# Optimization experiments

Hardware: AMD Instinct MI355X
Metric: run time of the kernel (lower is better)

## Reference

```python
import jax, jax.numpy as jnp
import numpy as np

IN_FEATURES = 4096
OUT_FEATURES = 16384
SCALE = 0.02


def setup_inputs() -> dict:
    key = jax.random.key(0)
    kx, kw, kb = jax.random.split(key, 3)
    x = jax.random.normal(kx, (4, 2048, IN_FEATURES), dtype=jnp.float32)
    # int8-valued quantized weight, stored as int32 (values in [-127, 127])
    q_weight = jax.random.randint(kw, (OUT_FEATURES, IN_FEATURES), -127, 128, dtype=jnp.int32)
    scale = jnp.float32(SCALE)
    bias = jax.random.normal(kb, (OUT_FEATURES,), dtype=jnp.float32)
    return {"x": x, "q_weight": q_weight, "scale": scale, "bias": bias}


def reference(x, q_weight, scale, bias):
    # weight = q_weight.float() * scale  (dequantize)
    weight = q_weight.astype(jnp.float32) * scale  # [out, in]
    # F.linear(x, weight, bias) = x @ weight.T + bias
    out = jnp.einsum('bsi,oi->bso', x, weight) + bias
    return out
```

## Files before the change

### kernel.cpp

```cpp
#include <hip/hip_runtime.h>
#include <stdint.h>

#define K_DIM 4096
#define N_DIM 16384
#define M_DIM 8192

typedef _Float16 half8 __attribute__((ext_vector_type(8)));
typedef float floatx4 __attribute__((ext_vector_type(4)));

__device__ inline void gld_lds16(const void* g, void* l) {
  __builtin_amdgcn_global_load_lds(
      (const __attribute__((address_space(1))) void*)g,
      (__attribute__((address_space(3))) void*)l, 16, 0, 0);
}

__global__ __launch_bounds__(256) void cvt_f32_f16_k(const float* __restrict__ in,
                                                     _Float16* __restrict__ out) {
  size_t idx = (size_t)blockIdx.x * 256 + threadIdx.x;
  const float4* p = (const float4*)in + idx * 2;
  float4 v0 = p[0], v1 = p[1];
  half8 h;
  h[0] = (_Float16)v0.x; h[1] = (_Float16)v0.y; h[2] = (_Float16)v0.z; h[3] = (_Float16)v0.w;
  h[4] = (_Float16)v1.x; h[5] = (_Float16)v1.y; h[6] = (_Float16)v1.z; h[7] = (_Float16)v1.w;
  *((half8*)out + idx) = h;
}

__global__ __launch_bounds__(256) void cvt_i32_f16_k(const int* __restrict__ in,
                                                     _Float16* __restrict__ out) {
  size_t idx = (size_t)blockIdx.x * 256 + threadIdx.x;
  const int4* p = (const int4*)in + idx * 2;
  int4 v0 = p[0], v1 = p[1];
  half8 h;
  h[0] = (_Float16)v0.x; h[1] = (_Float16)v0.y; h[2] = (_Float16)v0.z; h[3] = (_Float16)v0.w;
  h[4] = (_Float16)v1.x; h[5] = (_Float16)v1.y; h[6] = (_Float16)v1.z; h[7] = (_Float16)v1.w;
  *((half8*)out + idx) = h;
}

__global__ __launch_bounds__(512, 2) void qgemm256_k(
    const _Float16* __restrict__ Ah, const _Float16* __restrict__ Bh,
    const float* __restrict__ scale_p, const float* __restrict__ bias,
    float* __restrict__ out) {
  constexpr int BK = 64;
  constexpr int NT = K_DIM / BK;
  __shared__ __align__(16) _Float16 sA[2][256 * BK];
  __shared__ __align__(16) _Float16 sB[2][256 * BK];

  const int tid  = threadIdx.x;
  const int lane = tid & 63;
  const int wid  = tid >> 6;
  const int wm   = wid >> 2;
  const int wn   = wid & 3;
  const int q    = lane >> 4;
  const int l15  = lane & 15;

  const int nbn = N_DIM / 256;
  int lin = blockIdx.y * gridDim.x + blockIdx.x;
  int swz = (lin & 7) * ((M_DIM / 256) * nbn / 8) + (lin >> 3);
  const int bn = swz % nbn;
  const int bm = swz / nbn;

  const int s_slot = tid & 7;
  const int r0     = tid >> 3;
  const int cc     = s_slot ^ (r0 & 7);
  const _Float16* Agp = Ah + (size_t)(bm * 256 + r0) * K_DIM + cc * 8;
  const _Float16* Bgp = Bh + (size_t)(bn * 256 + r0) * K_DIM + cc * 8;

#define STAGE_A(b, tt, h)                                                        \
  { const _Float16* s_ = Agp + (size_t)(h) * 128 * K_DIM + (tt) * BK;            \
    gld_lds16(s_, &sA[(b)][(h) * 8192 + tid * 8]);                               \
    gld_lds16(s_ + (size_t)64 * K_DIM, &sA[(b)][(h) * 8192 + 4096 + tid * 8]); }
#define STAGE_B(b, tt, h)                                                        \
  { const _Float16* s_ = Bgp + (size_t)(h) * 128 * K_DIM + (tt) * BK;            \
    gld_lds16(s_, &sB[(b)][(h) * 8192 + tid * 8]);                               \
    gld_lds16(s_ + (size_t)64 * K_DIM, &sB[(b)][(h) * 8192 + 4096 + tid * 8]); }
#define MFMA16(d, a_, b_) d = __builtin_amdgcn_mfma_f32_16x16x32_f16(a_, b_, d, 0, 0, 0)
#define SBAR() __builtin_amdgcn_sched_barrier(0)
#define BARRIER() { SBAR(); __builtin_amdgcn_s_barrier(); SBAR(); }

  const int rbA = (wm * 128 + l15) * BK;
  const int rbB = (wn * 64 + l15) * BK;
  const int xt0 = (q ^ (l15 & 7)) * 8;
  const int xt1 = ((q + 4) ^ (l15 & 7)) * 8;

  floatx4 acc[8][4] = {};

  STAGE_A(0, 0, 0); STAGE_A(0, 0, 1);
  STAGE_B(0, 0, 0); STAGE_B(0, 0, 1);
  STAGE_A(1, 1, 0); STAGE_A(1, 1, 1);
  asm volatile("s_waitcnt vmcnt(4)" ::: "memory");
  BARRIER();

#pragma unroll 1
  for (int t = 0; t < NT; ++t) {
    const int buf = t & 1;
    const _Float16* pa = sA[buf];
    const _Float16* pb = sB[buf];
    half8 a0[8], a1[8], b0[4], b1[4];

    b0[0] = *(const half8*)&pb[rbB + xt0];
    b0[1] = *(const half8*)&pb[rbB + 1024 + xt0];
#pragma unroll
    for (int i = 0; i < 8; ++i) a0[i] = *(const half8*)&pa[rbA + i * 1024 + xt0];
    if (t < NT - 1) STAGE_B(buf ^ 1, t + 1, 0);
    BARRIER();
    __builtin_amdgcn_s_setprio(1);
#pragma unroll
    for (int i = 0; i < 8; ++i) { MFMA16(acc[i][0], a0[i], b0[0]); MFMA16(acc[i][1], a0[i], b0[1]); }
    __builtin_amdgcn_s_setprio(0);
    BARRIER();

    b0[2] = *(const half8*)&pb[rbB + 2048 + xt0];
    b0[3] = *(const half8*)&pb[rbB + 3072 + xt0];
#pragma unroll
    for (int i = 0; i < 8; ++i) a1[i] = *(const half8*)&pa[rbA + i * 1024 + xt1];
    if (t < NT - 1) STAGE_B(buf ^ 1, t + 1, 1);
    BARRIER();
    __builtin_amdgcn_s_setprio(1);
#pragma unroll
    for (int i = 0; i < 8; ++i) { MFMA16(acc[i][2], a0[i], b0[2]); MFMA16(acc[i][3], a0[i], b0[3]); }
    __builtin_amdgcn_s_setprio(0);
    BARRIER();

    b1[0] = *(const half8*)&pb[rbB + xt1];
    b1[1] = *(const half8*)&pb[rbB + 1024 + xt1];
    if (t < NT - 2) STAGE_A(buf, t + 2, 0);
    BARRIER();
    __builtin_amdgcn_s_setprio(1);
#pragma unroll
    for (int i = 0; i < 8; ++i) { MFMA16(acc[i][0], a1[i], b1[0]); MFMA16(acc[i][1], a1[i], b1[1]); }
    __builtin_amdgcn_s_setprio(0);
    BARRIER();

    b1[2] = *(const half8*)&pb[rbB + 2048 + xt1];
    b1[3] = *(const half8*)&pb[rbB + 3072 + xt1];
    if (t < NT - 2) STAGE_A(buf, t + 2, 1);
    BARRIER();
    __builtin_amdgcn_s_setprio(1);
#pragma unroll
    for (int i = 0; i < 8; ++i) { MFMA16(acc[i][2], a1[i], b1[2]); MFMA16(acc[i][3], a1[i], b1[3]); }
    __builtin_amdgcn_s_setprio(0);
    if (t < NT - 2) { asm volatile("s_waitcnt vmcnt(4)" ::: "memory"); }
    else            { asm volatile("s_waitcnt vmcnt(0)" ::: "memory"); }
    BARRIER();
  }

  const float s = *scale_p;
  float bv[4];
#pragma unroll
  for (int j = 0; j < 4; ++j) bv[j] = bias[bn * 256 + wn * 64 + j * 16 + l15];
  const int mb = bm * 256 + wm * 128 + q * 4;
  const size_t nb = (size_t)bn * 256 + wn * 64 + l15;
#pragma unroll
  for (int i = 0; i < 8; ++i) {
#pragma unroll
    for (int j = 0; j < 4; ++j) {
      size_t off = (size_t)(mb + i * 16) * N_DIM + nb + j * 16;
      floatx4 c = acc[i][j];
      out[off]             = c[0] * s + bv[j];
      out[off + N_DIM]     = c[1] * s + bv[j];
      out[off + 2 * N_DIM] = c[2] * s + bv[j];
      out[off + 3 * N_DIM] = c[3] * s + bv[j];
    }
  }
#undef STAGE_A
#undef STAGE_B
#undef MFMA16
#undef SBAR
#undef BARRIER
}

template <bool FROM_WS>
__global__ __launch_bounds__(256) void qgemm_k(const void* __restrict__ Av,
                                               const void* __restrict__ Bv,
                                               const float* __restrict__ scale_p,
                                               const float* __restrict__ bias,
                                               float* __restrict__ out) {
  constexpr int BK = 64;
  __shared__ __align__(16) _Float16 sA[128 * BK];
  __shared__ __align__(16) _Float16 sB[128 * BK];

  const int tid  = threadIdx.x;
  const int lane = tid & 63;
  const int wid  = tid >> 6;
  const int wm   = wid >> 1, wn = wid & 1;
  const int q    = lane >> 4;
  const int l15  = lane & 15;
  const int bn   = blockIdx.x, bm = blockIdx.y;

  int gI[4], rI[4], cI[4];
#pragma unroll
  for (int p = 0; p < 4; ++p) {
    int g = p * 256 + tid;
    gI[p] = g;
    rI[p] = g >> 3;
    cI[p] = (g & 7) ^ (rI[p] & 7);
  }

  floatx4 acc[4][4] = {};

  const int arow = wm * 64 + l15;
  const int brow = wn * 64 + l15;

  const _Float16* Ahp = nullptr; const _Float16* Bhp = nullptr;
  const float* Af = nullptr;     const int* Bq = nullptr;
  if constexpr (FROM_WS) { Ahp = (const _Float16*)Av; Bhp = (const _Float16*)Bv; }
  else                   { Af = (const float*)Av;     Bq = (const int*)Bv; }

#pragma unroll 1
  for (int k0 = 0; k0 < K_DIM; k0 += BK) {
    if constexpr (FROM_WS) {
#pragma unroll
      for (int p = 0; p < 4; ++p)
        gld_lds16(Ahp + (size_t)(bm * 128 + rI[p]) * K_DIM + k0 + cI[p] * 8, &sA[gI[p] * 8]);
#pragma unroll
      for (int p = 0; p < 4; ++p)
        gld_lds16(Bhp + (size_t)(bn * 128 + rI[p]) * K_DIM + k0 + cI[p] * 8, &sB[gI[p] * 8]);
    } else {
#pragma unroll
      for (int p = 0; p < 4; ++p) {
        const float4* pa =
            (const float4*)(Af + (size_t)(bm * 128 + rI[p]) * K_DIM + k0 + cI[p] * 8);
        float4 v0 = pa[0], v1 = pa[1];
        half8 h;
        h[0] = (_Float16)v0.x; h[1] = (_Float16)v0.y; h[2] = (_Float16)v0.z; h[3] = (_Float16)v0.w;
        h[4] = (_Float16)v1.x; h[5] = (_Float16)v1.y; h[6] = (_Float16)v1.z; h[7] = (_Float16)v1.w;
        *(half8*)&sA[gI[p] * 8] = h;
      }
#pragma unroll
      for (int p = 0; p < 4; ++p) {
        const int4* pb =
            (const int4*)(Bq + (size_t)(bn * 128 + rI[p]) * K_DIM + k0 + cI[p] * 8);
        int4 v0 = pb[0], v1 = pb[1];
        half8 h;
        h[0] = (_Float16)v0.x; h[1] = (_Float16)v0.y; h[2] = (_Float16)v0.z; h[3] = (_Float16)v0.w;
        h[4] = (_Float16)v1.x; h[5] = (_Float16)v1.y; h[6] = (_Float16)v1.z; h[7] = (_Float16)v1.w;
        *(half8*)&sB[gI[p] * 8] = h;
      }
    }
    __syncthreads();

#pragma unroll
    for (int kk = 0; kk < BK; kk += 32) {
      const int xt = ((((kk >> 3) + q) ^ (lane & 7)) * 8);
      half8 af[4], bf[4];
#pragma unroll
      for (int i = 0; i < 4; ++i) af[i] = *(const half8*)&sA[(arow + i * 16) * BK + xt];
#pragma unroll
      for (int j = 0; j < 4; ++j) bf[j] = *(const half8*)&sB[(brow + j * 16) * BK + xt];
#pragma unroll
      for (int i = 0; i < 4; ++i)
#pragma unroll
        for (int j = 0; j < 4; ++j)
          acc[i][j] = __builtin_amdgcn_mfma_f32_16x16x32_f16(af[i], bf[j], acc[i][j], 0, 0, 0);
    }
    __syncthreads();
  }

  const float s = *scale_p;
  float bv[4];
#pragma unroll
  for (int j = 0; j < 4; ++j) bv[j] = bias[bn * 128 + wn * 64 + j * 16 + l15];
  const int mb = bm * 128 + wm * 64 + q * 4;
  const size_t nb = (size_t)bn * 128 + wn * 64 + l15;
#pragma unroll
  for (int i = 0; i < 4; ++i) {
#pragma unroll
    for (int j = 0; j < 4; ++j) {
      size_t off = (size_t)(mb + i * 16) * N_DIM + nb + j * 16;
      floatx4 c = acc[i][j];
      out[off]             = c[0] * s + bv[j];
      out[off + N_DIM]     = c[1] * s + bv[j];
      out[off + 2 * N_DIM] = c[2] * s + bv[j];
      out[off + 3 * N_DIM] = c[3] * s + bv[j];
    }
  }
}

extern "C" void kernel_launch(void* const* d_in, const int* in_sizes, int n_in,
                              void* d_out, int out_size, void* d_ws, size_t ws_size,
                              hipStream_t stream) {
  const float* x     = (const float*)d_in[0];
  const int*   qw    = (const int*)d_in[1];
  const float* scale = (const float*)d_in[2];
  const float* bias  = (const float*)d_in[3];
  float* out = (float*)d_out;

  const size_t xs  = (size_t)M_DIM * K_DIM;
  const size_t wsz = (size_t)N_DIM * K_DIM;
  const size_t need = (xs + wsz) * sizeof(_Float16);

  if (ws_size >= need) {
    _Float16* xh = (_Float16*)d_ws;
    _Float16* wh = xh + xs;
    cvt_f32_f16_k<<<(int)(xs / 8 / 256), 256, 0, stream>>>(x, xh);
    cvt_i32_f16_k<<<(int)(wsz / 8 / 256), 256, 0, stream>>>(qw, wh);
    dim3 grid(N_DIM / 256, M_DIM / 256);
    qgemm256_k<<<grid, 512, 0, stream>>>(xh, wh, scale, bias, out);
  } else {
    dim3 grid(N_DIM / 128, M_DIM / 128);
    qgemm_k<false><<<grid, 256, 0, stream>>>(x, qw, scale, bias, out);
  }
}
```

Baseline: 1.827 ms.

## Restructure GEMM main loop into unrolled two-tile ping-pong with finer-grained staging

Unrolls the K loop by two so each half works on a fixed LDS buffer, and reorganizes the per-tile schedule. Each tile now issues all B fragment reads up front, splits A reads into quarter groups interleaved with 4x4 MFMA blocks, and spreads global-to-LDS staging of the next tiles across the phases using explicit lgkmcnt/vmcnt waits and raw s_barriers. The aim is better overlap of LDS reads, global loads and MFMA issue, and less scheduling overhead from sched_barriers. In exchange it holds more registers live and relies on hand-tuned wait counts, which could cause races or spills if the counts are wrong.

```diff
diff --git a/kernel.cpp b/kernel.cpp
--- a/kernel.cpp
+++ b/kernel.cpp
@@ -42,6 +42,7 @@
     float* __restrict__ out) {
   constexpr int BK = 64;
   constexpr int NT = K_DIM / BK;
+  constexpr int NI = NT / 2;
   __shared__ __align__(16) _Float16 sA[2][256 * BK];
   __shared__ __align__(16) _Float16 sB[2][256 * BK];
 
@@ -73,9 +74,23 @@
   { const _Float16* s_ = Bgp + (size_t)(h) * 128 * K_DIM + (tt) * BK;            \
     gld_lds16(s_, &sB[(b)][(h) * 8192 + tid * 8]);                               \
     gld_lds16(s_ + (size_t)64 * K_DIM, &sB[(b)][(h) * 8192 + 4096 + tid * 8]); }
-#define MFMA16(d, a_, b_) d = __builtin_amdgcn_mfma_f32_16x16x32_f16(a_, b_, d, 0, 0, 0)
-#define SBAR() __builtin_amdgcn_sched_barrier(0)
-#define BARRIER() { SBAR(); __builtin_amdgcn_s_barrier(); SBAR(); }
+#define MFMA_Q(i0, AARR, BARR)                                                   \
+  { _Pragma("unroll") for (int ii = 0; ii < 4; ++ii)                             \
+    _Pragma("unroll") for (int jj = 0; jj < 4; ++jj)                             \
+      acc[(i0) + ii][jj] = __builtin_amdgcn_mfma_f32_16x16x32_f16(               \
+          AARR[(i0) + ii], BARR[jj], acc[(i0) + ii][jj], 0, 0, 0); }
+#define RD_B4(arr, PB, XT)                                                       \
+  { _Pragma("unroll") for (int jj = 0; jj < 4; ++jj)                             \
+      arr[jj] = *(const half8*)&PB[rbB + jj * 1024 + (XT)]; }
+#define RD_A4(arr, i0, PA, XT)                                                   \
+  { _Pragma("unroll") for (int ii = 0; ii < 4; ++ii)                             \
+      arr[(i0) + ii] = *(const half8*)&PA[rbA + ((i0) + ii) * 1024 + (XT)]; }
+#define LGKM0()                                                                  \
+  { asm volatile("s_waitcnt lgkmcnt(0)" ::: "memory");                           \
+    __builtin_amdgcn_sched_barrier(0); }
+#define PRIO_MFMA(i0, AARR, BARR)                                                \
+  { __builtin_amdgcn_s_setprio(1); MFMA_Q(i0, AARR, BARR);                       \
+    __builtin_amdgcn_s_setprio(0); }
 
   const int rbA = (wm * 128 + l15) * BK;
   const int rbB = (wn * 64 + l15) * BK;
@@ -86,62 +101,82 @@
 
   STAGE_A(0, 0, 0); STAGE_A(0, 0, 1);
   STAGE_B(0, 0, 0); STAGE_B(0, 0, 1);
-  STAGE_A(1, 1, 0); STAGE_A(1, 1, 1);
-  asm volatile("s_waitcnt vmcnt(4)" ::: "memory");
-  BARRIER();
+  STAGE_B(1, 1, 0); STAGE_B(1, 1, 1);
+  STAGE_A(1, 1, 0);
+  asm volatile("s_waitcnt vmcnt(6)" ::: "memory");
+  __builtin_amdgcn_s_barrier();
 
 #pragma unroll 1
-  for (int t = 0; t < NT; ++t) {
-    const int buf = t & 1;
-    const _Float16* pa = sA[buf];
-    const _Float16* pb = sB[buf];
+  for (int i = 0; i < NI; ++i) {
+    const int t0 = 2 * i;
+    const bool more = (i < NI - 1);
     half8 a0[8], a1[8], b0[4], b1[4];
 
-    b0[0] = *(const half8*)&pb[rbB + xt0];
-    b0[1] = *(const half8*)&pb[rbB + 1024 + xt0];
-#pragma unroll
-    for (int i = 0; i < 8; ++i) a0[i] = *(const half8*)&pa[rbA + i * 1024 + xt0];
-    if (t < NT - 1) STAGE_B(buf ^ 1, t + 1, 0);
-    BARRIER();
-    __builtin_amdgcn_s_setprio(1);
-#pragma unroll
-    for (int i = 0; i < 8; ++i) { MFMA16(acc[i][0], a0[i], b0[0]); MFMA16(acc[i][1], a0[i], b0[1]); }
-    __builtin_amdgcn_s_setprio(0);
-    BARRIER();
-
-    b0[2] = *(const half8*)&pb[rbB + 2048 + xt0];
-    b0[3] = *(const half8*)&pb[rbB + 3072 + xt0];
-#pragma unroll
-    for (int i = 0; i < 8; ++i) a1[i] = *(const half8*)&pa[rbA + i * 1024 + xt1];
-    if (t < NT - 1) STAGE_B(buf ^ 1, t + 1, 1);
-    BARRIER();
-    __builtin_amdgcn_s_setprio(1);
-#pragma unroll
-    for (int i = 0; i < 8; ++i) { MFMA16(acc[i][2], a0[i], b0[2]); MFMA16(acc[i][3], a0[i], b0[3]); }
-    __builtin_amdgcn_s_setprio(0);
-    BARRIER();
-
-    b1[0] = *(const half8*)&pb[rbB + xt1];
-    b1[1] = *(const half8*)&pb[rbB + 1024 + xt1];
-    if (t < NT - 2) STAGE_A(buf, t + 2, 0);
-    BARRIER();
-    __builtin_amdgcn_s_setprio(1);
-#pragma unroll
-    for (int i = 0; i < 8; ++i) { MFMA16(acc[i][0], a1[i], b1[0]); MFMA16(acc[i][1], a1[i], b1[1]); }
-    __builtin_amdgcn_s_setprio(0);
-    BARRIER();
-
-    b1[2] = *(const half8*)&pb[rbB + 2048 + xt1];
-    b1[3] = *(const half8*)&pb[rbB + 3072 + xt1];
-    if (t < NT - 2) STAGE_A(buf, t + 2, 1);
-    BARRIER();
-    __builtin_amdgcn_s_setprio(1);
-#pragma unroll
-    for (int i = 0; i < 8; ++i) { MFMA16(acc[i][2], a1[i], b1[2]); MFMA16(acc[i][3], a1[i], b1[3]); }
-    __builtin_amdgcn_s_setprio(0);
-    if (t < NT - 2) { asm volatile("s_waitcnt vmcnt(4)" ::: "memory"); }
-    else            { asm volatile("s_waitcnt vmcnt(0)" ::: "memory"); }
-    BARRIER();
+    {
+      const _Float16* pa = sA[0];
+      const _Float16* pb = sB[0];
+      RD_B4(b0, pb, xt0);
+      RD_B4(b1, pb, xt1);
+      RD_A4(a0, 0, pa, xt0);
+      STAGE_A(1, t0 + 1, 1);
+      asm volatile("s_waitcnt lgkmcnt(8)" ::: "memory");
+      __builtin_amdgcn_s_barrier();
+      LGKM0();
+      PRIO_MFMA(0, a0, b0);
+      __builtin_amdgcn_s_barrier();
+      RD_A4(a0, 4, pa, xt0);
+      RD_A4(a1, 0, pa, xt1);
+      if (more) STAGE_B(0, t0 + 2, 0);
+      __builtin_amdgcn_s_barrier();
+      LGKM0();
+      PRIO_MFMA(4, a0, b0);
+      __builtin_amdgcn_s_barrier();
+      RD_A4(a1, 4, pa, xt1);
+      if (more) STAGE_B(0, t0 + 2, 1);
+      __builtin_amdgcn_s_barrier();
+      LGKM0();
+      PRIO_MFMA(0, a1, b1);
+      __builtin_amdgcn_s_barrier();
+      if (more) STAGE_A(0, t0 + 2, 0);
+      __builtin_amdgcn_s_barrier();
+      PRIO_MFMA(4, a1, b1);
+      if (more) { asm volatile("s_waitcnt vmcnt(6)" ::: "memory"); }
+      else      { asm volatile("s_waitcnt vmcnt(0)" ::: "memory"); }
+      __builtin_amdgcn_s_barrier();
+    }
+
+    {
+      const _Float16* pa = sA[1];
+      const _Float16* pb = sB[1];
+      RD_B4(b0, pb, xt0);
+      RD_B4(b1, pb, xt1);
+      RD_A4(a0, 0, pa, xt0);
+      if (more) STAGE_A(0, t0 + 2, 1);
+      asm volatile("s_waitcnt lgkmcnt(8)" ::: "memory");
+      __builtin_amdgcn_s_barrier();
+      LGKM0();
+      PRIO_MFMA(0, a0, b0);
+      __builtin_amdgcn_s_barrier();
+      RD_A4(a0, 4, pa, xt0);
+      RD_A4(a1, 0, pa, xt1);
+      if (more) STAGE_B(1, t0 + 3, 0);
+      __builtin_amdgcn_s_barrier();
+      LGKM0();
+      PRIO_MFMA(4, a0, b0);
+      __builtin_amdgcn_s_barrier();
+      RD_A4(a1, 4, pa, xt1);
+      if (more) STAGE_B(1, t0 + 3, 1);
+      __builtin_amdgcn_s_barrier();
+      LGKM0();
+      PRIO_MFMA(0, a1, b1);
+      __builtin_amdgcn_s_barrier();
+      if (more) STAGE_A(1, t0 + 3, 0);
+      __builtin_amdgcn_s_barrier();
+      PRIO_MFMA(4, a1, b1);
+      if (more) { asm volatile("s_waitcnt vmcnt(6)" ::: "memory"); }
+      else      { asm volatile("s_waitcnt vmcnt(0)" ::: "memory"); }
+      __builtin_amdgcn_s_barrier();
+    }
   }
 
   const float s = *scale_p;
@@ -164,9 +199,11 @@
   }
 #undef STAGE_A
 #undef STAGE_B
-#undef MFMA16
-#undef SBAR
-#undef BARRIER
+#undef MFMA_Q
+#undef RD_B4
+#undef RD_A4
+#undef LGKM0
+#undef PRIO_MFMA
 }
 
 template <bool FROM_WS>
```

Result: faster. 1.787 ms (-2.2%).
